# Performance work log

Hardware: AMD Instinct MI355X
Metric: run time of the kernel (lower is better)

The kernel has to match this reference:

```python
import jax, jax.numpy as jnp
import numpy as np

EMBED = 1024
HEADS = 16
HEAD_DIM = EMBED // HEADS
DIVIDER = int(np.sqrt(HEAD_DIM))  # torch code uses int(sqrt(head_dim)) == 8


def setup_inputs() -> dict:
    key = jax.random.key(0)
    ks = jax.random.split(key, 9)
    B, S = 2, 2048
    scale = 1.0 / np.sqrt(EMBED)
    def lin(kw, kb):
        W = jax.random.uniform(kw, (EMBED, EMBED), jnp.float32, -scale, scale)
        b = jax.random.uniform(kb, (EMBED,), jnp.float32, -scale, scale)
        return W, b
    Wq, bq = lin(ks[0], ks[1])
    Wk, bk = lin(ks[2], ks[3])
    Wv, bv = lin(ks[4], ks[5])
    Wo, bo = lin(ks[6], ks[7])
    x = jax.random.normal(ks[8], (B, S, EMBED), jnp.float32)
    return {"x": x, "Wq": Wq, "bq": bq, "Wk": Wk, "bk": bk,
            "Wv": Wv, "bv": bv, "Wo": Wo, "bo": bo}


def reference(x, Wq, bq, Wk, bk, Wv, bv, Wo, bo):
    B, S, _ = x.shape
    # projections (torch Linear: x @ W.T + b)
    q = x @ Wq.T + bq
    k = x @ Wk.T + bk
    v = x @ Wv.T + bv
    # split heads: [B, S, H, D] -> [B, H, S, D]
    def heads(t):
        return t.reshape(B, S, HEADS, HEAD_DIM).transpose(0, 2, 1, 3)
    q, k, v = heads(q), heads(k), heads(v)
    # scores [B, H, S, S]
    scores = jnp.einsum('bhsd,bhtd->bhst', q, k) / DIVIDER
    attn = jax.nn.softmax(scores, axis=-1)
    out = jnp.einsum('bhst,bhtd->bhsd', attn, v)
    out = out.transpose(0, 2, 1, 3).reshape(B, S, EMBED)
    return out @ Wo.T + bo
```

## Files before the change

kernel.cpp:

```cpp
#include <hip/hip_runtime.h>
#include <hip/hip_bf16.h>
#include <stdint.h>

using bf16 = __hip_bfloat16;
typedef __attribute__((ext_vector_type(8))) short   short8;
typedef __attribute__((ext_vector_type(4))) float   floatx4;
typedef __attribute__((ext_vector_type(2))) unsigned int uint2v;

static __device__ __forceinline__ unsigned short f2bf(float f) {
    return __builtin_bit_cast(unsigned short, __float2bfloat16(f));
}

static __device__ __forceinline__ uint4 load8bf(const void* p, size_t e, int f) {
    if (!f) return *(const uint4*)((const ushort*)p + e);
    const float* fp = (const float*)p + e;
    float4 a = *(const float4*)fp;
    float4 b = *(const float4*)(fp + 4);
    union { uint4 u; unsigned short s[8]; } r;
    r.s[0] = f2bf(a.x); r.s[1] = f2bf(a.y); r.s[2] = f2bf(a.z); r.s[3] = f2bf(a.w);
    r.s[4] = f2bf(b.x); r.s[5] = f2bf(b.y); r.s[6] = f2bf(b.z); r.s[7] = f2bf(b.w);
    return r.u;
}
static __device__ __forceinline__ float loadScalar(const void* p, int i, int f) {
    return f ? ((const float*)p)[i] : __bfloat162float(((const bf16*)p)[i]);
}

__global__ void detect_dtype(const ushort* __restrict__ x, int* __restrict__ flag) {
    __shared__ int cnt;
    if (threadIdx.x == 0) cnt = 0;
    __syncthreads();
    unsigned short u = x[threadIdx.x * 2];
    int e = (u >> 7) & 0xFF;
    int bad = (e > 133 || e < 94) ? 1 : 0;
    atomicAdd(&cnt, bad);
    __syncthreads();
    if (threadIdx.x == 0) *flag = (cnt > 64) ? 1 : 0;
}

template<int BM>
__global__ __launch_bounds__(512, 4)
void gemm_bt(const void* __restrict__ A,
             const void* __restrict__ Wa, const void* __restrict__ Wb,
             const void* __restrict__ Ba, const void* __restrict__ Bb,
             void* __restrict__ Oa, void* __restrict__ Ob_,
             int pa, int pb, int a_ext, int out_ext,
             const int* __restrict__ flagp)
{
    constexpr int MB = BM / 128;
    constexpr int P  = BM / 64;
    constexpr int SG = BM / 8;
    __shared__ ushort pool[BM * 64 + 4096];

    const int f  = *flagp;
    const int fA = a_ext ? f : 0;
    const int z  = blockIdx.z;
    const void* W   = z ? Wb : Wa;
    const void* Bi  = z ? Bb : Ba;
    void*       Out = z ? Ob_ : Oa;
    const int   pm  = z ? pb : pa;

    const int m0 = blockIdx.x * BM;
    const int n0 = blockIdx.y * 64;
    const int tid  = threadIdx.x;
    const int lane = tid & 63;
    const int wave = tid >> 6;
    const int r15  = lane & 15;
    const int quad = lane >> 4;

    const int srow = tid >> 3;
    const int sg   = tid & 7;

    ushort* xs  = pool;
    ushort* wsm = pool + BM * 64;

    floatx4 acc[MB][4];
#pragma unroll
    for (int mb = 0; mb < MB; mb++)
#pragma unroll
        for (int db = 0; db < 4; db++) acc[mb][db] = (floatx4){0.f, 0.f, 0.f, 0.f};

    uint4 apre[P], wpre;
#pragma unroll
    for (int p = 0; p < P; p++)
        apre[p] = load8bf(A, (size_t)(m0 + srow + p * 64) * 1024 + sg * 8, fA);
    wpre = load8bf(W, (size_t)(n0 + srow) * 1024 + sg * 8, f);

    for (int kb = 0; kb < 1024; kb += 64) {
#pragma unroll
        for (int p = 0; p < P; p++) {
            int row = srow + p * 64;
            *(uint4*)(&xs[row * 64 + ((sg ^ (row & 7)) << 3)]) = apre[p];
        }
        *(uint4*)(&wsm[srow * 64 + ((sg ^ (srow & 7)) << 3)]) = wpre;
        __syncthreads();
        if (kb + 64 < 1024) {
#pragma unroll
            for (int p = 0; p < P; p++)
                apre[p] = load8bf(A, (size_t)(m0 + srow + p * 64) * 1024
                                      + kb + 64 + sg * 8, fA);
            wpre = load8bf(W, (size_t)(n0 + srow) * 1024 + kb + 64 + sg * 8, f);
        }
#pragma unroll
        for (int ks = 0; ks < 2; ks++) {
            short8 af[MB];
#pragma unroll
            for (int mb = 0; mb < MB; mb++) {
                int arow = wave * (16 * MB) + mb * 16 + r15;
                af[mb] = *(const short8*)(
                    &xs[arow * 64 + (((ks * 4 + quad) ^ (arow & 7)) << 3)]);
            }
#pragma unroll
            for (int db = 0; db < 4; db++) {
                int brow = db * 16 + r15;
                short8 bv = *(const short8*)(
                    &wsm[brow * 64 + (((ks * 4 + quad) ^ (brow & 7)) << 3)]);
#pragma unroll
                for (int mb = 0; mb < MB; mb++)
                    acc[mb][db] = __builtin_amdgcn_mfma_f32_16x16x32_bf16(
                        af[mb], bv, acc[mb][db], 0, 0, 0);
            }
        }
        __syncthreads();
    }

    if (pm == 2) {
#pragma unroll
        for (int mb = 0; mb < MB; mb++)
#pragma unroll
            for (int db = 0; db < 4; db++) {
                int d = db * 16 + r15;
                float bias = loadScalar(Bi, n0 + d, f);
                int s4 = wave * (16 * MB) + mb * 16 + quad * 4;
                union { uint2 u; ushort us[4]; } pk;
#pragma unroll
                for (int r = 0; r < 4; r++) pk.us[r] = f2bf(acc[mb][db][r] + bias);
                *(uint2*)(&pool[d * BM + (((s4 >> 3) ^ (d & 15)) << 3) + (s4 & 7)])
                    = pk.u;
            }
        __syncthreads();
        const int b_  = m0 >> 11;
        const int h   = n0 >> 6;
        const int sl0 = m0 & 2047;
#pragma unroll
        for (int rr = 0; rr < (64 * SG) / 512; rr++) {
            int idx = rr * 512 + tid;
            int d = idx / SG, sgrp = idx % SG;
            uint4 v = *(const uint4*)(&pool[d * BM + ((sgrp ^ (d & 15)) << 3)]);
            *(uint4*)((ushort*)Out +
                      ((size_t)((b_ * 16 + h) * 64 + d) << 11) + sl0 + sgrp * 8) = v;
        }
        return;
    }

#pragma unroll
    for (int mb = 0; mb < MB; mb++)
#pragma unroll
        for (int db = 0; db < 4; db++) {
            int col = n0 + db * 16 + r15;
            float bias = loadScalar(Bi, col, f);
#pragma unroll
            for (int r = 0; r < 4; r++) {
                int row = m0 + wave * (16 * MB) + mb * 16 + quad * 4 + r;
                float v = acc[mb][db][r] + bias;
                if (pm == 1) {
                    int hh = col >> 6, d = col & 63;
                    int b_ = row >> 11, s = row & 2047;
                    ((ushort*)Out)[(((size_t)(b_ * 16 + hh) * 2048 + s) << 6) + d]
                        = f2bf(v);
                } else if (out_ext && f) {
                    ((float*)Out)[(size_t)row * 1024 + col] = v;
                } else {
                    ((ushort*)Out)[(size_t)row * 1024 + col] = f2bf(v);
                }
            }
        }
}

__global__ __launch_bounds__(512, 4)
void attn_fused(const void* __restrict__ x, const void* __restrict__ Wq,
                const void* __restrict__ bq,
                const ushort* __restrict__ K, const ushort* __restrict__ VT,
                ushort* __restrict__ AO, const int* __restrict__ flagp)
{
    __shared__ ushort pool[24576];

    const int f   = *flagp;
    const int bh  = blockIdx.x;
    const int h   = bh & 15, b_ = bh >> 4;
    const int q0  = blockIdx.y * 128;
    const int tid  = threadIdx.x;
    const int lane = tid & 63;
    const int wave = tid >> 6;
    const int r15  = lane & 15;
    const int quad = lane >> 4;
    const size_t base = (size_t)bh << 17;

    const int srow = tid >> 3;
    const int sg   = tid & 7;

    uint4 kpre = *(const uint4*)(K  + base + (size_t)srow * 64   + sg * 8);
    uint4 vpre = *(const uint4*)(VT + base + (size_t)srow * 2048 + sg * 8);

    floatx4 qacc[4];
#pragma unroll
    for (int db = 0; db < 4; db++) qacc[db] = (floatx4){0.f,0.f,0.f,0.f};

    uint4 xpre[2], wpre;
#pragma unroll
    for (int p = 0; p < 2; p++)
        xpre[p] = load8bf(x, (size_t)(b_ * 2048 + q0 + srow + p * 64) * 1024
                              + sg * 8, f);
    wpre = load8bf(Wq, (size_t)(h * 64 + srow) * 1024 + sg * 8, f);

    for (int kb = 0; kb < 1024; kb += 64) {
        int buf = (kb >> 6) & 1;
        ushort* xs  = pool + buf * 8192;
        ushort* wsm = pool + 16384 + buf * 4096;
#pragma unroll
        for (int p = 0; p < 2; p++) {
            int row = srow + p * 64;
            *(uint4*)(&xs[row * 64 + ((sg ^ (row & 7)) << 3)]) = xpre[p];
        }
        *(uint4*)(&wsm[srow * 64 + ((sg ^ (srow & 7)) << 3)]) = wpre;
        __syncthreads();
        if (kb + 64 < 1024) {
#pragma unroll
            for (int p = 0; p < 2; p++)
                xpre[p] = load8bf(x, (size_t)(b_ * 2048 + q0 + srow + p * 64) * 1024
                                      + kb + 64 + sg * 8, f);
            wpre = load8bf(Wq, (size_t)(h * 64 + srow) * 1024 + kb + 64 + sg * 8, f);
        }
#pragma unroll
        for (int ks = 0; ks < 2; ks++) {
            int arow = wave * 16 + r15;
            short8 af = *(const short8*)(
                &xs[arow * 64 + (((ks * 4 + quad) ^ (arow & 7)) << 3)]);
#pragma unroll
            for (int db = 0; db < 4; db++) {
                int brow = db * 16 + r15;
                short8 bv = *(const short8*)(
                    &wsm[brow * 64 + (((ks * 4 + quad) ^ (brow & 7)) << 3)]);
                qacc[db] = __builtin_amdgcn_mfma_f32_16x16x32_bf16(
                    af, bv, qacc[db], 0, 0, 0);
            }
        }
    }

    ushort* Qs = pool;
    const float csc = 0.1803368801f;
#pragma unroll
    for (int db = 0; db < 4; db++) {
        int d = db * 16 + r15;
        float bias = loadScalar(bq, h * 64 + d, f);
#pragma unroll
        for (int r = 0; r < 4; r++) {
            int q = wave * 16 + quad * 4 + r;
            Qs[q * 64 + (((d >> 3) ^ (q & 7)) << 3) + (d & 7)] =
                f2bf((qacc[db][r] + bias) * csc);
        }
    }
    short8 qf[2];
#pragma unroll
    for (int ks = 0; ks < 2; ks++) {
        int arow = wave * 16 + r15;
        qf[ks] = *(const short8*)(
            &Qs[arow * 64 + (((ks * 4 + quad) ^ (arow & 7)) << 3)]);
    }
    __syncthreads();

    floatx4 oacc[4], lacc;
#pragma unroll
    for (int db = 0; db < 4; db++) oacc[db] = (floatx4){0.f,0.f,0.f,0.f};
    lacc = (floatx4){0.f,0.f,0.f,0.f};
    short8 ones;
#pragma unroll
    for (int j = 0; j < 8; j++) ones[j] = (short)0x3F80;

    for (int t0 = 0; t0 < 2048; t0 += 64) {
        int buf = (t0 >> 6) & 1;
        ushort* Ks = pool + buf * 4096;
        ushort* Vt = pool + 8192 + buf * 4096;
        *(uint4*)(&Ks[srow * 64 + ((sg ^ (srow & 7)) << 3)]) = kpre;
        *(uint4*)(&Vt[srow * 64 + ((sg ^ (srow & 7)) << 3)]) = vpre;
        __syncthreads();
        if (t0 < 1984) {
            kpre = *(const uint4*)(K  + base + (size_t)(t0 + 64 + srow) * 64
                                       + sg * 8);
            vpre = *(const uint4*)(VT + base + (size_t)srow * 2048
                                       + t0 + 64 + sg * 8);
        }

        floatx4 s[4];
#pragma unroll
        for (int mb = 0; mb < 4; mb++) s[mb] = (floatx4){0.f,0.f,0.f,0.f};
#pragma unroll
        for (int ks = 0; ks < 2; ks++)
#pragma unroll
            for (int mb = 0; mb < 4; mb++) {
                int arow = mb * 16 + r15;
                short8 kf = *(const short8*)(
                    &Ks[arow * 64 + (((ks * 4 + quad) ^ (arow & 7)) << 3)]);
                s[mb] = __builtin_amdgcn_mfma_f32_16x16x32_bf16(
                    kf, qf[ks], s[mb], 0, 0, 0);
            }

        uint Lr[4], Hr[4];
#pragma unroll
        for (int mb = 0; mb < 4; mb++) {
            uint b0 = __builtin_bit_cast(uint, __builtin_amdgcn_exp2f(s[mb][0]));
            uint b1 = __builtin_bit_cast(uint, __builtin_amdgcn_exp2f(s[mb][1]));
            uint b2 = __builtin_bit_cast(uint, __builtin_amdgcn_exp2f(s[mb][2]));
            uint b3 = __builtin_bit_cast(uint, __builtin_amdgcn_exp2f(s[mb][3]));
            Lr[mb] = (b1 & 0xFFFF0000u) | (b0 >> 16);
            Hr[mb] = (b3 & 0xFFFF0000u) | (b2 >> 16);
        }
        short8 pf[2];
#pragma unroll
        for (int ks2 = 0; ks2 < 2; ks2++) {
            uint2v tL = __builtin_amdgcn_permlane32_swap(
                Lr[ks2 * 2], Lr[ks2 * 2 + 1], false, false);
            uint2v uL = __builtin_amdgcn_permlane16_swap(
                tL[0], tL[1], false, false);
            uint2v tH = __builtin_amdgcn_permlane32_swap(
                Hr[ks2 * 2], Hr[ks2 * 2 + 1], false, false);
            uint2v uH = __builtin_amdgcn_permlane16_swap(
                tH[0], tH[1], false, false);
            union { uint u[4]; short8 s8; } pk;
            pk.u[0] = uL[0]; pk.u[1] = uH[0]; pk.u[2] = uL[1]; pk.u[3] = uH[1];
            pf[ks2] = pk.s8;
        }

#pragma unroll
        for (int ks2 = 0; ks2 < 2; ks2++) {
#pragma unroll
            for (int db = 0; db < 4; db++) {
                int brow = db * 16 + r15;
                short8 vf = *(const short8*)(
                    &Vt[brow * 64 + (((ks2 * 4 + quad) ^ (brow & 7)) << 3)]);
                oacc[db] = __builtin_amdgcn_mfma_f32_16x16x32_bf16(
                    pf[ks2], vf, oacc[db], 0, 0, 0);
            }
            lacc = __builtin_amdgcn_mfma_f32_16x16x32_bf16(
                pf[ks2], ones, lacc, 0, 0, 0);
        }
    }

    float inv[4];
#pragma unroll
    for (int r = 0; r < 4; r++) inv[r] = 1.f / lacc[r];
#pragma unroll
    for (int db = 0; db < 4; db++) {
        int d = db * 16 + r15;
#pragma unroll
        for (int r = 0; r < 4; r++) {
            int qi = q0 + wave * 16 + quad * 4 + r;
            AO[((size_t)(b_ * 2048 + qi) << 10) + h * 64 + d] =
                f2bf(oacc[db][r] * inv[r]);
        }
    }
}

__global__ void copy_u4(const uint4* __restrict__ src, uint4* __restrict__ dst) {
    size_t i = (size_t)blockIdx.x * 256 + threadIdx.x;
    dst[i] = src[i];
}

extern "C" void kernel_launch(void* const* d_in, const int* in_sizes, int n_in,
                              void* d_out, int out_size, void* d_ws, size_t ws_size,
                              hipStream_t stream)
{
    const void* x  = d_in[0];
    const void* Wq = d_in[1];
    const void* bq = d_in[2];
    const void* Wk = d_in[3];
    const void* bk = d_in[4];
    const void* Wv = d_in[5];
    const void* bv = d_in[6];
    const void* Wo = d_in[7];
    const void* bo = d_in[8];

    const size_t TEN = (size_t)2 * 16 * 2048 * 64;
    int*    flagp = (int*)d_ws;
    ushort* Kw    = (ushort*)((char*)d_ws + 256);
    ushort* Vw    = Kw + TEN;
    const bool big_ws = ws_size >= 3 * TEN * sizeof(ushort) + 256;
    ushort* AOw   = big_ws ? (Vw + TEN) : (ushort*)d_out;
    ushort* Oin   = big_ws ? AOw : Kw;

    detect_dtype<<<1, 256, 0, stream>>>((const ushort*)x, flagp);

    gemm_bt<128><<<dim3(32, 16, 2), dim3(512), 0, stream>>>(
        x, Wk, Wv, bk, bv, Kw, Vw, 1, 2, 1,
        0, flagp);

    attn_fused<<<dim3(32, 16), dim3(512), 0, stream>>>(
        x, Wq, bq, Kw, Vw, AOw, flagp);

    if (!big_ws)
        copy_u4<<<dim3(2048), dim3(256), 0, stream>>>(
            (const uint4*)d_out, (uint4*)Oin);

    gemm_bt<128><<<dim3(32, 16, 1), dim3(512), 0, stream>>>(
        Oin, Wo, Wo, bo, bo, d_out, d_out, 0, 0, 0,
        1, flagp);
}
```

Baseline: 228.2 us.

## Split key tile across wave pairs, each wave handling 32 queries

Reorganizes attention work so each wave computes 32 query rows against half of each 64-key tile (split-K over keys), instead of 16 queries against the full tile. Each K fragment loaded from LDS is reused across two query blocks and each V fragment across two P fragments, cutting LDS reads per MFMA. The two key-halves' partial output and row-sum accumulators are then combined through shared memory at the end. This costs more accumulator registers, an extra reduction with two barriers, and leaves half the waves idle during the final write.

Result: no change. 224.1 us (-1.8%).

```diff
diff --git a/kernel.cpp b/kernel.cpp
--- a/kernel.cpp
+++ b/kernel.cpp
@@ -191,6 +191,8 @@
     const int tid  = threadIdx.x;
     const int lane = tid & 63;
     const int wave = tid >> 6;
+    const int qg   = wave >> 1;
+    const int kh   = wave & 1;
     const int r15  = lane & 15;
     const int quad = lane >> 4;
     const size_t base = (size_t)bh << 17;
@@ -259,19 +261,25 @@
                 f2bf((qacc[db][r] + bias) * csc);
         }
     }
-    short8 qf[2];
-#pragma unroll
-    for (int ks = 0; ks < 2; ks++) {
-        int arow = wave * 16 + r15;
-        qf[ks] = *(const short8*)(
-            &Qs[arow * 64 + (((ks * 4 + quad) ^ (arow & 7)) << 3)]);
-    }
     __syncthreads();
-
-    floatx4 oacc[4], lacc;
-#pragma unroll
-    for (int db = 0; db < 4; db++) oacc[db] = (floatx4){0.f,0.f,0.f,0.f};
-    lacc = (floatx4){0.f,0.f,0.f,0.f};
+    short8 qf2[2][2];
+#pragma unroll
+    for (int qb = 0; qb < 2; qb++)
+#pragma unroll
+        for (int ks = 0; ks < 2; ks++) {
+            int arow = qg * 32 + qb * 16 + r15;
+            qf2[qb][ks] = *(const short8*)(
+                &Qs[arow * 64 + (((ks * 4 + quad) ^ (arow & 7)) << 3)]);
+        }
+    __syncthreads();
+
+    floatx4 oacc[2][4], lacc[2];
+#pragma unroll
+    for (int qb = 0; qb < 2; qb++) {
+#pragma unroll
+        for (int db = 0; db < 4; db++) oacc[qb][db] = (floatx4){0.f,0.f,0.f,0.f};
+        lacc[qb] = (floatx4){0.f,0.f,0.f,0.f};
+    }
     short8 ones;
 #pragma unroll
     for (int j = 0; j < 8; j++) ones[j] = (short)0x3F80;
@@ -290,72 +298,106 @@
                                        + t0 + 64 + sg * 8);
         }
 
-        floatx4 s[4];
-#pragma unroll
-        for (int mb = 0; mb < 4; mb++) s[mb] = (floatx4){0.f,0.f,0.f,0.f};
+        floatx4 s[2][2];
+#pragma unroll
+        for (int mb = 0; mb < 2; mb++)
+#pragma unroll
+            for (int qb = 0; qb < 2; qb++) s[mb][qb] = (floatx4){0.f,0.f,0.f,0.f};
 #pragma unroll
         for (int ks = 0; ks < 2; ks++)
 #pragma unroll
-            for (int mb = 0; mb < 4; mb++) {
-                int arow = mb * 16 + r15;
+            for (int mb = 0; mb < 2; mb++) {
+                int arow = kh * 32 + mb * 16 + r15;
                 short8 kf = *(const short8*)(
                     &Ks[arow * 64 + (((ks * 4 + quad) ^ (arow & 7)) << 3)]);
-                s[mb] = __builtin_amdgcn_mfma_f32_16x16x32_bf16(
-                    kf, qf[ks], s[mb], 0, 0, 0);
-            }
-
-        uint Lr[4], Hr[4];
-#pragma unroll
-        for (int mb = 0; mb < 4; mb++) {
-            uint b0 = __builtin_bit_cast(uint, __builtin_amdgcn_exp2f(s[mb][0]));
-            uint b1 = __builtin_bit_cast(uint, __builtin_amdgcn_exp2f(s[mb][1]));
-            uint b2 = __builtin_bit_cast(uint, __builtin_amdgcn_exp2f(s[mb][2]));
-            uint b3 = __builtin_bit_cast(uint, __builtin_amdgcn_exp2f(s[mb][3]));
-            Lr[mb] = (b1 & 0xFFFF0000u) | (b0 >> 16);
-            Hr[mb] = (b3 & 0xFFFF0000u) | (b2 >> 16);
-        }
+#pragma unroll
+                for (int qb = 0; qb < 2; qb++)
+                    s[mb][qb] = __builtin_amdgcn_mfma_f32_16x16x32_bf16(
+                        kf, qf2[qb][ks], s[mb][qb], 0, 0, 0);
+            }
+
+        uint Lr[2][2], Hr[2][2];
+#pragma unroll
+        for (int mb = 0; mb < 2; mb++)
+#pragma unroll
+            for (int qb = 0; qb < 2; qb++) {
+                uint b0 = __builtin_bit_cast(uint, __builtin_amdgcn_exp2f(s[mb][qb][0]));
+                uint b1 = __builtin_bit_cast(uint, __builtin_amdgcn_exp2f(s[mb][qb][1]));
+                uint b2 = __builtin_bit_cast(uint, __builtin_amdgcn_exp2f(s[mb][qb][2]));
+                uint b3 = __builtin_bit_cast(uint, __builtin_amdgcn_exp2f(s[mb][qb][3]));
+                Lr[mb][qb] = (b1 & 0xFFFF0000u) | (b0 >> 16);
+                Hr[mb][qb] = (b3 & 0xFFFF0000u) | (b2 >> 16);
+            }
         short8 pf[2];
 #pragma unroll
-        for (int ks2 = 0; ks2 < 2; ks2++) {
+        for (int qb = 0; qb < 2; qb++) {
             uint2v tL = __builtin_amdgcn_permlane32_swap(
-                Lr[ks2 * 2], Lr[ks2 * 2 + 1], false, false);
+                Lr[0][qb], Lr[1][qb], false, false);
             uint2v uL = __builtin_amdgcn_permlane16_swap(
                 tL[0], tL[1], false, false);
             uint2v tH = __builtin_amdgcn_permlane32_swap(
-                Hr[ks2 * 2], Hr[ks2 * 2 + 1], false, false);
+                Hr[0][qb], Hr[1][qb], false, false);
             uint2v uH = __builtin_amdgcn_permlane16_swap(
                 tH[0], tH[1], false, false);
             union { uint u[4]; short8 s8; } pk;
             pk.u[0] = uL[0]; pk.u[1] = uH[0]; pk.u[2] = uL[1]; pk.u[3] = uH[1];
-            pf[ks2] = pk.s8;
-        }
-
-#pragma unroll
-        for (int ks2 = 0; ks2 < 2; ks2++) {
-#pragma unroll
-            for (int db = 0; db < 4; db++) {
-                int brow = db * 16 + r15;
-                short8 vf = *(const short8*)(
-                    &Vt[brow * 64 + (((ks2 * 4 + quad) ^ (brow & 7)) << 3)]);
-                oacc[db] = __builtin_amdgcn_mfma_f32_16x16x32_bf16(
-                    pf[ks2], vf, oacc[db], 0, 0, 0);
-            }
-            lacc = __builtin_amdgcn_mfma_f32_16x16x32_bf16(
-                pf[ks2], ones, lacc, 0, 0, 0);
-        }
-    }
-
-    float inv[4];
-#pragma unroll
-    for (int r = 0; r < 4; r++) inv[r] = 1.f / lacc[r];
-#pragma unroll
-    for (int db = 0; db < 4; db++) {
-        int d = db * 16 + r15;
-#pragma unroll
-        for (int r = 0; r < 4; r++) {
-            int qi = q0 + wave * 16 + quad * 4 + r;
-            AO[((size_t)(b_ * 2048 + qi) << 10) + h * 64 + d] =
-                f2bf(oacc[db][r] * inv[r]);
+            pf[qb] = pk.s8;
+        }
+
+#pragma unroll
+        for (int db = 0; db < 4; db++) {
+            int brow = db * 16 + r15;
+            short8 vf = *(const short8*)(
+                &Vt[brow * 64 + (((kh * 4 + quad) ^ (brow & 7)) << 3)]);
+#pragma unroll
+            for (int qb = 0; qb < 2; qb++)
+                oacc[qb][db] = __builtin_amdgcn_mfma_f32_16x16x32_bf16(
+                    pf[qb], vf, oacc[qb][db], 0, 0, 0);
+        }
+#pragma unroll
+        for (int qb = 0; qb < 2; qb++)
+            lacc[qb] = __builtin_amdgcn_mfma_f32_16x16x32_bf16(
+                pf[qb], ones, lacc[qb], 0, 0, 0);
+    }
+
+    __syncthreads();
+    {
+        char* rb = (char*)pool + qg * 10240 + lane * 16;
+        if (kh) {
+#pragma unroll
+            for (int qb = 0; qb < 2; qb++) {
+#pragma unroll
+                for (int db = 0; db < 4; db++)
+                    *(floatx4*)(rb + (qb * 4 + db) * 1024) = oacc[qb][db];
+                *(floatx4*)(rb + (8 + qb) * 1024) = lacc[qb];
+            }
+        }
+        __syncthreads();
+        if (!kh) {
+#pragma unroll
+            for (int qb = 0; qb < 2; qb++) {
+#pragma unroll
+                for (int db = 0; db < 4; db++)
+                    oacc[qb][db] += *(const floatx4*)(rb + (qb * 4 + db) * 1024);
+                lacc[qb] += *(const floatx4*)(rb + (8 + qb) * 1024);
+            }
+            float inv[2][4];
+#pragma unroll
+            for (int qb = 0; qb < 2; qb++)
+#pragma unroll
+                for (int r = 0; r < 4; r++) inv[qb][r] = 1.f / lacc[qb][r];
+#pragma unroll
+            for (int qb = 0; qb < 2; qb++)
+#pragma unroll
+                for (int db = 0; db < 4; db++) {
+                    int d = db * 16 + r15;
+#pragma unroll
+                    for (int r = 0; r < 4; r++) {
+                        int qi = q0 + qg * 32 + qb * 16 + quad * 4 + r;
+                        AO[((size_t)(b_ * 2048 + qi) << 10) + h * 64 + d] =
+                            f2bf(oacc[qb][db][r] * inv[qb][r]);
+                    }
+                }
         }
     }
 }
```
